# Kernel optimization log

Measured on AMD Instinct MI355X. Metric: run time of the kernel, lower is better.

Reference implementation:

```python
import jax, jax.numpy as jnp
import numpy as np

E = 128          # embed_dim / d_model
DI = 2 * E       # d_inner = expand * d_model = 256
H = 8            # nheads = d_inner / headdim
P = 32           # headdim
N = 64           # d_state
DC = 4           # d_conv
G = 1            # ngroups
XBC = DI + 2 * G * N            # 384
DIN = 2 * DI + 2 * G * N + H    # 648 in_proj width
NL = 4           # number of Mamba2 blocks
PS = 16          # patch size
EPS = 1e-5


def _silu(x):
    return x * jax.nn.sigmoid(x)


def _ln(x, w, b):
    mu = jnp.mean(x, axis=-1, keepdims=True)
    var = jnp.mean(jnp.square(x - mu), axis=-1, keepdims=True)
    return (x - mu) * jax.lax.rsqrt(var + EPS) * w + b


def setup_inputs() -> dict:
    key = jax.random.key(0)
    ks = jax.random.split(key, 20)
    B, IMG = 256, 256
    s = 0.02
    inp = {
        "x": jax.random.normal(ks[0], (B, 3, IMG, IMG), jnp.float32),
        # patch embed conv (E, 3, PS, PS) + bias, then LayerNorm
        "conv_w": jax.random.normal(ks[1], (E, 3, PS, PS), jnp.float32) * s,
        "conv_b": jnp.zeros((E,), jnp.float32),
        "pe_ln_w": jnp.ones((E,), jnp.float32),
        "pe_ln_b": jnp.zeros((E,), jnp.float32),
        # per-block LayerNorms (stacked over NL layers)
        "ln_w": jnp.ones((NL, E), jnp.float32),
        "ln_b": jnp.zeros((NL, E), jnp.float32),
        # Mamba2 params stacked over layers
        "in_w": jax.random.normal(ks[2], (NL, DIN, E), jnp.float32) * s,
        "conv1d_w": jax.random.normal(ks[3], (NL, XBC, DC), jnp.float32) * s,
        "conv1d_b": jnp.zeros((NL, XBC), jnp.float32),
        "dt_bias": jax.random.normal(ks[4], (NL, H), jnp.float32) * 0.5,
        "A_log": jnp.tile(jnp.log(jnp.arange(1, H + 1, dtype=jnp.float32)), (NL, 1)),
        "Dp": jnp.ones((NL, H), jnp.float32),
        "ssm_norm_w": jnp.ones((NL, DI), jnp.float32),
        "out_w": jax.random.normal(ks[5], (NL, E, DI), jnp.float32) * s,
        # final norm + head
        "fn_w": jnp.ones((E,), jnp.float32),
        "fn_b": jnp.zeros((E,), jnp.float32),
        "head_w": jax.random.normal(ks[6], (128, E), jnp.float32) * s,
        "head_b": jnp.zeros((128,), jnp.float32),
    }
    return inp


def _mamba2(x, in_w, cw, cb, dtb, A_log, Dp, nw, ow):
    B, L, _ = x.shape
    zxbcdt = jnp.einsum('ble,de->bld', x, in_w)          # [B,L,648]
    z = zxbcdt[..., :DI]                                  # [B,L,256]
    xbc = zxbcdt[..., DI:DI + XBC]                        # [B,L,384]
    dt = jax.nn.softplus(zxbcdt[..., DI + XBC:] + dtb)    # [B,L,H]
    # causal depthwise conv1d over seq, kernel DC, + silu
    xp = jnp.pad(xbc, ((0, 0), (DC - 1, 0), (0, 0)))
    conv = cb + sum(cw[:, k] * xp[:, k:k + L, :] for k in range(DC))
    xbc = _silu(conv)
    xh = xbc[..., :DI].reshape(B, L, H, P)                # [B,L,H,P]
    Bm = xbc[..., DI:DI + N]                              # [B,L,N] (g=1)
    Cm = xbc[..., DI + N:]                                # [B,L,N]
    A = -jnp.exp(A_log)                                   # [H]
    dA = jnp.exp(dt * A)                                  # [B,L,H]
    # sequential selective scan over L
    def step(h, t):
        dAt, dtt, xt, Bt, Ct = t
        h = dAt[..., None, None] * h + (dtt[..., None] * xt)[..., None] * Bt[:, None, None, :]
        y = jnp.einsum('bhpn,bn->bhp', h, Ct)
        return h, y
    h0 = jnp.zeros((B, H, P, N), x.dtype)
    xs = (jnp.moveaxis(dA, 1, 0), jnp.moveaxis(dt, 1, 0), jnp.moveaxis(xh, 1, 0),
          jnp.moveaxis(Bm, 1, 0), jnp.moveaxis(Cm, 1, 0))
    _, ys = jax.lax.scan(step, h0, xs)                    # [L,B,H,P]
    y = jnp.moveaxis(ys, 0, 1) + Dp[:, None] * xh         # [B,L,H,P]
    y = y.reshape(B, L, DI)
    # gated RMSNorm: rmsnorm(y * silu(z)) * weight
    y = y * _silu(z)
    y = y * jax.lax.rsqrt(jnp.mean(jnp.square(y), axis=-1, keepdims=True) + EPS) * nw
    return jnp.einsum('bld,ed->ble', y, ow)


def reference(x, conv_w, conv_b, pe_ln_w, pe_ln_b, ln_w, ln_b, in_w, conv1d_w,
              conv1d_b, dt_bias, A_log, Dp, ssm_norm_w, out_w, fn_w, fn_b,
              head_w, head_b):
    B = x.shape[0]
    Hh = x.shape[2] // PS
    Ww = x.shape[3] // PS
    # non-overlapping patch conv == blocked einsum
    xp = x.reshape(B, 3, Hh, PS, Ww, PS)
    t = jnp.einsum('bcxpyq,ecpq->bxye', xp, conv_w) + conv_b
    t = t.reshape(B, Hh * Ww, E)                          # [B,L,E]
    t = _ln(t, pe_ln_w, pe_ln_b)
    for i in range(NL):
        t = t + _mamba2(_ln(t, ln_w[i], ln_b[i]), in_w[i], conv1d_w[i],
                        conv1d_b[i], dt_bias[i], A_log[i], Dp[i],
                        ssm_norm_w[i], out_w[i])
    t = _ln(t, fn_w, fn_b)
    t = jnp.mean(t, axis=1)                               # [B,E]
    t = jnp.einsum('be,oe->bo', t, head_w) + head_b       # [B,128]
    nrm = jnp.maximum(jnp.linalg.norm(t, axis=1, keepdims=True), 1e-12)
    return t / nrm
```

## Files before the change

kernel.cpp:

```cpp
#include <hip/hip_runtime.h>
#include <math.h>

#define EE 128
#define DI 256
#define HH 8
#define PP 32
#define NN 64
#define DC 4
#define XBC 384
#define DIN 648
#define NL 4
#define LSEQ 256
#define BB 256
#define TTOK (BB * LSEQ)
#define EPSF 1e-5f

typedef __attribute__((ext_vector_type(8))) short short8;
typedef __attribute__((ext_vector_type(4))) float f32x4;

__device__ inline short f2bf(float f) {
  unsigned u = __builtin_bit_cast(unsigned, f);
  u += 0x7fff + ((u >> 16) & 1);
  return (short)(u >> 16);
}
__device__ inline float bf2f(unsigned short u) {
  unsigned x = ((unsigned)u) << 16;
  return __builtin_bit_cast(float, x);
}
__device__ inline float fast_silu(float a) {
  return a * __builtin_amdgcn_rcpf(1.f + __expf(-a));
}

__global__ __launch_bounds__(256) void cvt_w_kernel(
    const float* __restrict__ in_w, const float* __restrict__ ow,
    unsigned short* __restrict__ in_wb, unsigned short* __restrict__ owb) {
  int i = blockIdx.x * 256 + threadIdx.x;
  in_wb[i] = (unsigned short)f2bf(in_w[i]);
  if (i < NL * EE * DI) owb[i] = (unsigned short)f2bf(ow[i]);
}

__global__ __launch_bounds__(256) void gemm_in_proj(
    const unsigned short* __restrict__ A, const unsigned short* __restrict__ B,
    const unsigned short* __restrict__ Wdt,
    unsigned short* __restrict__ Czx, float* __restrict__ dtraw) {
  __shared__ __align__(16) unsigned short As[128][136];
  __shared__ __align__(16) unsigned short Bs[128][136];
  const int tid = threadIdx.x;
  const int lane = tid & 63, wid = tid >> 6;
  const int wm = wid >> 1, wn = wid & 1;
  const int m0 = blockIdx.y * 128, n0 = blockIdx.x * 128;
  const int r = tid >> 1, hf = tid & 1;
  const int lr = lane & 15, lk = (lane >> 4) * 8;
  {
    const unsigned short* ap = A + (size_t)(m0 + r) * 128 + hf * 64;
#pragma unroll
    for (int v = 0; v < 8; ++v)
      *(short8*)&As[r][hf * 64 + v * 8] = *(const short8*)(ap + v * 8);
    const unsigned short* bp = B + (size_t)(n0 + r) * 128 + hf * 64;
#pragma unroll
    for (int v = 0; v < 8; ++v)
      *(short8*)&Bs[r][hf * 64 + v * 8] = *(const short8*)(bp + v * 8);
  }
  __syncthreads();
  f32x4 acc[4][4] = {};
#pragma unroll
  for (int ks = 0; ks < 4; ++ks) {
    int k0 = ks * 32;
    short8 af[4], bfr[4];
#pragma unroll
    for (int mi = 0; mi < 4; ++mi) af[mi] = *(const short8*)&As[wm * 64 + mi * 16 + lr][k0 + lk];
#pragma unroll
    for (int ni = 0; ni < 4; ++ni) bfr[ni] = *(const short8*)&Bs[wn * 64 + ni * 16 + lr][k0 + lk];
#pragma unroll
    for (int mi = 0; mi < 4; ++mi)
#pragma unroll
      for (int ni = 0; ni < 4; ++ni)
        acc[mi][ni] = __builtin_amdgcn_mfma_f32_16x16x32_bf16(af[mi], bfr[ni], acc[mi][ni], 0, 0, 0);
  }
  if (n0 == 0) {
    f32x4 accd[2] = {};
#pragma unroll
    for (int ks = 0; ks < 4; ++ks) {
      int k0 = ks * 32;
      short8 bw = {};
      if (lr < 8) bw = *(const short8*)(Wdt + (size_t)lr * 128 + k0 + lk);
#pragma unroll
      for (int f = 0; f < 2; ++f) {
        short8 av = *(const short8*)&As[wid * 32 + f * 16 + lr][k0 + lk];
        accd[f] = __builtin_amdgcn_mfma_f32_16x16x32_bf16(av, bw, accd[f], 0, 0, 0);
      }
    }
    if (lr < 8) {
#pragma unroll
      for (int f = 0; f < 2; ++f) {
        int row0 = m0 + wid * 32 + f * 16 + (lane >> 4) * 4;
#pragma unroll
        for (int j = 0; j < 4; ++j)
          dtraw[(size_t)(row0 + j) * 8 + lr] = accd[f][j];
      }
    }
  }
  __syncthreads();
  {
    unsigned short (*Vt)[136] = (unsigned short(*)[136])&As[0][0];
#pragma unroll
    for (int mi = 0; mi < 4; ++mi) {
#pragma unroll
      for (int ni = 0; ni < 4; ++ni) {
        int row0 = wm * 64 + mi * 16 + (lane >> 4) * 4;
        int col = wn * 64 + ni * 16 + lr;
#pragma unroll
        for (int j = 0; j < 4; ++j)
          Vt[row0 + j][col] = (unsigned short)f2bf(acc[mi][ni][j]);
      }
    }
    __syncthreads();
    const int row = tid >> 4, cs = (tid & 15) * 8;
#pragma unroll
    for (int it = 0; it < 8; ++it) {
      int rr2 = it * 16 + row;
      *(uint4*)(Czx + (size_t)(m0 + rr2) * DIN + n0 + cs) = *(const uint4*)&Vt[rr2][cs];
    }
  }
}

__global__ __launch_bounds__(256) void gemm_out_fused_ln(
    const unsigned short* __restrict__ ysc, const unsigned short* __restrict__ zx,
    const float* __restrict__ nw, const unsigned short* __restrict__ B,
    unsigned short* __restrict__ tres, const float* __restrict__ lnw,
    const float* __restrict__ lnb, unsigned* __restrict__ tnb) {
  __shared__ short As[128][40];
  __shared__ short Bs[128][40];
  __shared__ unsigned short Vt[128][136];
  __shared__ float rs_g[128], mu_s[128], rs_s[128];
  const int tid = threadIdx.x;
  const int lane = tid & 63, wid = tid >> 6;
  const int wm = wid >> 1, wn = wid & 1;
  const int m0 = blockIdx.x * 128;
  const int r = tid >> 1, hf = tid & 1;
  const int lr = lane & 15, lk = (lane >> 4) * 8;
  f32x4 acc[4][4] = {};
  float ssg = 0.f;
  for (int k0 = 0; k0 < 256; k0 += 32) {
    {
      int col = k0 + hf * 16;
      const unsigned short* yp = ysc + (size_t)(m0 + r) * DI + col;
      const unsigned short* zp = zx + (size_t)(m0 + r) * DIN + col;
      short8 y0 = *(const short8*)(yp);
      short8 y1 = *(const short8*)(yp + 8);
      short8 z0 = *(const short8*)(zp);
      short8 z1 = *(const short8*)(zp + 8);
      float4 nw0 = *(const float4*)(nw + col);
      float4 nw1 = *(const float4*)(nw + col + 4);
      float4 nw2 = *(const float4*)(nw + col + 8);
      float4 nw3 = *(const float4*)(nw + col + 12);
      float nwv[16] = {nw0.x, nw0.y, nw0.z, nw0.w, nw1.x, nw1.y, nw1.z, nw1.w,
                       nw2.x, nw2.y, nw2.z, nw2.w, nw3.x, nw3.y, nw3.z, nw3.w};
      short8 a0, a1;
#pragma unroll
      for (int j = 0; j < 8; ++j) {
        float y = bf2f((unsigned short)y0[j]);
        float z = bf2f((unsigned short)z0[j]);
        float g = y * fast_silu(z);
        ssg += g * g;
        a0[j] = f2bf(g * nwv[j]);
        float y2 = bf2f((unsigned short)y1[j]);
        float z2 = bf2f((unsigned short)z1[j]);
        float g2 = y2 * fast_silu(z2);
        ssg += g2 * g2;
        a1[j] = f2bf(g2 * nwv[8 + j]);
      }
      *(short8*)&As[r][hf * 16] = a0;
      *(short8*)&As[r][hf * 16 + 8] = a1;
    }
    {
      const unsigned short* bp = B + (size_t)r * 256 + k0 + hf * 16;
      *(short8*)&Bs[r][hf * 16] = *(const short8*)(bp);
      *(short8*)&Bs[r][hf * 16 + 8] = *(const short8*)(bp + 8);
    }
    __syncthreads();
    short8 af[4], bfr[4];
#pragma unroll
    for (int mi = 0; mi < 4; ++mi) af[mi] = *(const short8*)&As[wm * 64 + mi * 16 + lr][lk];
#pragma unroll
    for (int ni = 0; ni < 4; ++ni) bfr[ni] = *(const short8*)&Bs[wn * 64 + ni * 16 + lr][lk];
#pragma unroll
    for (int mi = 0; mi < 4; ++mi)
#pragma unroll
      for (int ni = 0; ni < 4; ++ni)
        acc[mi][ni] = __builtin_amdgcn_mfma_f32_16x16x32_bf16(af[mi], bfr[ni], acc[mi][ni], 0, 0, 0);
    __syncthreads();
  }
  ssg += __shfl_xor(ssg, 1);
  if (hf == 0) rs_g[r] = rsqrtf(ssg * (1.f / 256.f) + EPSF);
  __syncthreads();
#pragma unroll
  for (int mi = 0; mi < 4; ++mi) {
#pragma unroll
    for (int ni = 0; ni < 4; ++ni) {
      int row0 = wm * 64 + mi * 16 + (lane >> 4) * 4;
      int col = wn * 64 + ni * 16 + lr;
#pragma unroll
      for (int j = 0; j < 4; ++j) {
        int row = row0 + j;
        size_t idx = (size_t)(m0 + row) * 128 + col;
        float v = acc[mi][ni][j] * rs_g[row] + bf2f(tres[idx]);
        unsigned short us = (unsigned short)f2bf(v);
        tres[idx] = us;
        Vt[row][col] = us;
      }
    }
  }
  __syncthreads();
  {
    float s = 0.f, ss = 0.f;
#pragma unroll
    for (int kk = 0; kk < 8; ++kk) {
      short8 vv = *(const short8*)&Vt[r][hf * 64 + kk * 8];
#pragma unroll
      for (int j = 0; j < 8; ++j) {
        float f = bf2f((unsigned short)vv[j]);
        s += f; ss += f * f;
      }
    }
    s += __shfl_xor(s, 1);
    ss += __shfl_xor(ss, 1);
    if (hf == 0) {
      float mu = s * (1.f / 128.f);
      mu_s[r] = mu;
      rs_s[r] = rsqrtf(ss * (1.f / 128.f) - mu * mu + EPSF);
    }
  }
  __syncthreads();
  float w0 = lnw[lane * 2], w1 = lnw[lane * 2 + 1];
  float b0 = lnb[lane * 2], b1 = lnb[lane * 2 + 1];
  for (int it = 0; it < 32; ++it) {
    int row = it * 4 + wid;
    float mu = mu_s[row], rr = rs_s[row];
    float v0 = bf2f(Vt[row][lane * 2]);
    float v1 = bf2f(Vt[row][lane * 2 + 1]);
    unsigned lo = (unsigned short)f2bf((v0 - mu) * rr * w0 + b0);
    unsigned hi = (unsigned short)f2bf((v1 - mu) * rr * w1 + b1);
    tnb[(size_t)(m0 + row) * 64 + lane] = lo | (hi << 16);
  }
}

__global__ __launch_bounds__(256) void gemm_bf16_patch(
    const float* __restrict__ X, const float* __restrict__ B,
    const float* __restrict__ bias, unsigned short* __restrict__ C) {
  __shared__ short As[128][40];
  __shared__ short Bs[128][40];
  const int tid = threadIdx.x;
  const int lane = tid & 63, wid = tid >> 6;
  const int wm = wid >> 1, wn = wid & 1;
  const int m0 = blockIdx.x * 128;
  const int r = tid >> 1, hf = tid & 1;
  const int lr = lane & 15, lk = (lane >> 4) * 8;
  const int m = m0 + r;
  const int bb = m >> 8, px = (m >> 4) & 15, py = m & 15;
  f32x4 acc[4][4] = {};
  for (int k0 = 0; k0 < 768; k0 += 32) {
    int k = k0 + hf * 16;
    int c = k >> 8, dx = (k >> 4) & 15;
    {
      const float* ap = X + (((size_t)(bb * 3 + c) * 256 + px * 16 + dx) * 256 + py * 16);
      float4 v0 = *(const float4*)(ap + 0);
      float4 v1 = *(const float4*)(ap + 4);
      float4 v2 = *(const float4*)(ap + 8);
      float4 v3 = *(const float4*)(ap + 12);
      short8 s0, s1;
      s0[0] = f2bf(v0.x); s0[1] = f2bf(v0.y); s0[2] = f2bf(v0.z); s0[3] = f2bf(v0.w);
      s0[4] = f2bf(v1.x); s0[5] = f2bf(v1.y); s0[6] = f2bf(v1.z); s0[7] = f2bf(v1.w);
      s1[0] = f2bf(v2.x); s1[1] = f2bf(v2.y); s1[2] = f2bf(v2.z); s1[3] = f2bf(v2.w);
      s1[4] = f2bf(v3.x); s1[5] = f2bf(v3.y); s1[6] = f2bf(v3.z); s1[7] = f2bf(v3.w);
      *(short8*)&As[r][hf * 16] = s0;
      *(short8*)&As[r][hf * 16 + 8] = s1;
    }
    {
      const float* bp = B + (size_t)r * 768 + k;
      float4 v0 = *(const float4*)(bp + 0);
      float4 v1 = *(const float4*)(bp + 4);
      float4 v2 = *(const float4*)(bp + 8);
      float4 v3 = *(const float4*)(bp + 12);
      short8 s0, s1;
      s0[0] = f2bf(v0.x); s0[1] = f2bf(v0.y); s0[2] = f2bf(v0.z); s0[3] = f2bf(v0.w);
      s0[4] = f2bf(v1.x); s0[5] = f2bf(v1.y); s0[6] = f2bf(v1.z); s0[7] = f2bf(v1.w);
      s1[0] = f2bf(v2.x); s1[1] = f2bf(v2.y); s1[2] = f2bf(v2.z); s1[3] = f2bf(v2.w);
      s1[4] = f2bf(v3.x); s1[5] = f2bf(v3.y); s1[6] = f2bf(v3.z); s1[7] = f2bf(v3.w);
      *(short8*)&Bs[r][hf * 16] = s0;
      *(short8*)&Bs[r][hf * 16 + 8] = s1;
    }
    __syncthreads();
    short8 af[4], bfr[4];
#pragma unroll
    for (int mi = 0; mi < 4; ++mi) af[mi] = *(const short8*)&As[wm * 64 + mi * 16 + lr][lk];
#pragma unroll
    for (int ni = 0; ni < 4; ++ni) bfr[ni] = *(const short8*)&Bs[wn * 64 + ni * 16 + lr][lk];
#pragma unroll
    for (int mi = 0; mi < 4; ++mi)
#pragma unroll
      for (int ni = 0; ni < 4; ++ni)
        acc[mi][ni] = __builtin_amdgcn_mfma_f32_16x16x32_bf16(af[mi], bfr[ni], acc[mi][ni], 0, 0, 0);
    __syncthreads();
  }
#pragma unroll
  for (int mi = 0; mi < 4; ++mi) {
#pragma unroll
    for (int ni = 0; ni < 4; ++ni) {
      int row0 = m0 + wm * 64 + mi * 16 + (lane >> 4) * 4;
      int col = wn * 64 + ni * 16 + (lane & 15);
#pragma unroll
      for (int j = 0; j < 4; ++j)
        C[(size_t)(row0 + j) * 128 + col] = (unsigned short)f2bf(acc[mi][ni][j] + bias[col]);
    }
  }
}

__global__ __launch_bounds__(256) void ln_pe0_kernel(
    unsigned* t, unsigned* out,
    const float* __restrict__ pe_w, const float* __restrict__ pe_b,
    const float* __restrict__ l0w, const float* __restrict__ l0b) {
  int wid = threadIdx.x >> 6, lane = threadIdx.x & 63;
  size_t token = (size_t)blockIdx.x * 4 + wid;
  unsigned* p = t + token * 64;
  unsigned u = p[lane];
  float vx = bf2f((unsigned short)(u & 0xffff));
  float vy = bf2f((unsigned short)(u >> 16));
  float s = vx + vy;
#pragma unroll
  for (int off = 1; off < 64; off <<= 1) s += __shfl_xor(s, off);
  float mu = s * (1.f / 128.f);
  float dx = vx - mu, dy = vy - mu;
  float vs = dx * dx + dy * dy;
#pragma unroll
  for (int off = 1; off < 64; off <<= 1) vs += __shfl_xor(vs, off);
  float r = rsqrtf(vs * (1.f / 128.f) + EPSF);
  float t0 = dx * r * pe_w[lane * 2 + 0] + pe_b[lane * 2 + 0];
  float t1 = dy * r * pe_w[lane * 2 + 1] + pe_b[lane * 2 + 1];
  unsigned short s0 = (unsigned short)f2bf(t0);
  unsigned short s1 = (unsigned short)f2bf(t1);
  p[lane] = (unsigned)s0 | ((unsigned)s1 << 16);
  float r0 = bf2f(s0), r1 = bf2f(s1);
  float s2 = r0 + r1;
#pragma unroll
  for (int off = 1; off < 64; off <<= 1) s2 += __shfl_xor(s2, off);
  float mu2 = s2 * (1.f / 128.f);
  float d0 = r0 - mu2, d1 = r1 - mu2;
  float vs2 = d0 * d0 + d1 * d1;
#pragma unroll
  for (int off = 1; off < 64; off <<= 1) vs2 += __shfl_xor(vs2, off);
  float r2 = rsqrtf(vs2 * (1.f / 128.f) + EPSF);
  unsigned lo = (unsigned short)f2bf(d0 * r2 * l0w[lane * 2 + 0] + l0b[lane * 2 + 0]);
  unsigned hi = (unsigned short)f2bf(d1 * r2 * l0w[lane * 2 + 1] + l0b[lane * 2 + 1]);
  out[token * 64 + lane] = lo | (hi << 16);
}

__global__ __launch_bounds__(256, 2) void scan_chunk_kernel(
    const unsigned short* __restrict__ zx,
    const float* __restrict__ dtraw,
    const float* __restrict__ dtb,
    const float* __restrict__ A_log,
    const float* __restrict__ cw,
    const float* __restrict__ cbv_g,
    const float* __restrict__ Dp,
    unsigned short* __restrict__ ysc) {
  const int b = blockIdx.x & 255, hq = blockIdx.x >> 8;
  const int h0 = hq * 4;
  const int tid = threadIdx.x;
  const int w = tid >> 6, lane = tid & 63;
  const int lr = lane & 15, lj = lane >> 4;
  __shared__ __align__(16) unsigned short Cb[64][72];
  __shared__ __align__(16) unsigned short Bb[64][72];
  __shared__ __align__(16) unsigned short BbT[64][72];
  __shared__ __align__(16) unsigned short Pb[64][72];
  __shared__ __align__(16) unsigned short xT[4][32][72];
  __shared__ __align__(16) unsigned short hbT[4][32][72];
  __shared__ float la[4][64], dtc[4][64], wt[4][64];
  for (int i = tid; i < 4608; i += 256) ((unsigned*)hbT)[i] = 0;
  f32x4 acc_h[8] = {};
  const float dp0 = Dp[h0], dp1 = Dp[h0 + 1], dp2 = Dp[h0 + 2], dp3 = Dp[h0 + 3];
  __syncthreads();

  for (int c = 0; c < 4; ++c) {
    const int tok0 = b * 256 + c * 64;
    {
      int hh = h0 + w;
      float raw = dtraw[(size_t)(tok0 + lane) * 8 + hh] + dtb[hh];
      float dt = raw > 20.f ? raw : log1pf(expf(raw));
      float v = -expf(A_log[hh]) * dt;
#pragma unroll
      for (int off = 1; off < 64; off <<= 1) {
        float u = __shfl_up(v, off);
        if (lane >= off) v += u;
      }
      la[w][lane] = v;
      dtc[w][lane] = dt;
    }
    for (int it = tid; it < 512; it += 256) {
      int t0, ch, kind, sub;
      if (it < 256) {
        int hx = it >> 6, id = it & 63;
        t0 = (id >> 2) * 4; sub = (id & 3) * 8;
        ch = (h0 + hx) * 32 + sub; kind = hx;
      } else if (it < 384) {
        int id = it - 256;
        t0 = (id >> 3) * 4; sub = (id & 7) * 8;
        ch = 256 + sub; kind = 4;
      } else {
        int id = it - 384;
        t0 = (id >> 3) * 4; sub = (id & 7) * 8;
        ch = 320 + sub; kind = 5;
      }
      const unsigned short* zp = zx + (size_t)(tok0 + t0) * DIN + 256 + ch;
      const int t0loc = c * 64 + t0;
      short8 rr[7];
      if (t0loc >= 3) {
#pragma unroll
        for (int d = 0; d < 7; ++d)
          rr[d] = *(const short8*)(zp + (ptrdiff_t)(d - 3) * DIN);
      } else {
#pragma unroll
        for (int d = 0; d < 7; ++d) {
          short8 z8 = {};
          if (t0loc + d - 3 >= 0) z8 = *(const short8*)(zp + (ptrdiff_t)(d - 3) * DIN);
          rr[d] = z8;
        }
      }
      float4 cwv[8];
      float cbl[8];
#pragma unroll
      for (int j = 0; j < 8; ++j) {
        cwv[j] = *(const float4*)(cw + (ch + j) * 4);
        cbl[j] = cbv_g[ch + j];
      }
      short8 o[4];
#pragma unroll
      for (int tt = 0; tt < 4; ++tt) {
#pragma unroll
        for (int j = 0; j < 8; ++j) {
          float a = cbl[j]
                  + cwv[j].x * bf2f((unsigned short)rr[tt + 0][j])
                  + cwv[j].y * bf2f((unsigned short)rr[tt + 1][j])
                  + cwv[j].z * bf2f((unsigned short)rr[tt + 2][j])
                  + cwv[j].w * bf2f((unsigned short)rr[tt + 3][j]);
          o[tt][j] = f2bf(fast_silu(a));
        }
      }
      if (kind < 4) {
#pragma unroll
        for (int j = 0; j < 8; ++j) {
          ushort4 v;
          v.x = (unsigned short)o[0][j]; v.y = (unsigned short)o[1][j];
          v.z = (unsigned short)o[2][j]; v.w = (unsigned short)o[3][j];
          *(ushort4*)&xT[kind][sub + j][t0] = v;
        }
      } else if (kind == 4) {
        *(short8*)&Bb[t0 + 0][sub] = o[0];
        *(short8*)&Bb[t0 + 1][sub] = o[1];
        *(short8*)&Bb[t0 + 2][sub] = o[2];
        *(short8*)&Bb[t0 + 3][sub] = o[3];
#pragma unroll
        for (int j = 0; j < 8; ++j) {
          ushort4 v;
          v.x = (unsigned short)o[0][j]; v.y = (unsigned short)o[1][j];
          v.z = (unsigned short)o[2][j]; v.w = (unsigned short)o[3][j];
          *(ushort4*)&BbT[sub + j][t0] = v;
        }
      } else {
        *(short8*)&Cb[t0 + 0][sub] = o[0];
        *(short8*)&Cb[t0 + 1][sub] = o[1];
        *(short8*)&Cb[t0 + 2][sub] = o[2];
        *(short8*)&Cb[t0 + 3][sub] = o[3];
      }
    }
    __syncthreads();
    wt[w][lane] = __expf(la[w][63] - la[w][lane]) * dtc[w][lane];
    short8 afC0 = *(const short8*)&Cb[w * 16 + lr][lj * 8];
    short8 afC1 = *(const short8*)&Cb[w * 16 + lr][32 + lj * 8];
    f32x4 acc_s[4] = {};
#pragma unroll
    for (int ni = 0; ni < 4; ++ni) {
      short8 bf0 = *(const short8*)&Bb[ni * 16 + lr][lj * 8];
      short8 bf1 = *(const short8*)&Bb[ni * 16 + lr][32 + lj * 8];
      acc_s[ni] = __builtin_amdgcn_mfma_f32_16x16x32_bf16(afC0, bf0, acc_s[ni], 0, 0, 0);
      acc_s[ni] = __builtin_amdgcn_mfma_f32_16x16x32_bf16(afC1, bf1, acc_s[ni], 0, 0, 0);
    }
    f32x4 acc_y[4][2] = {};
#pragma unroll
    for (int hh = 0; hh < 4; ++hh) {
#pragma unroll
      for (int ni = 0; ni < 2; ++ni) {
        short8 hf0 = *(const short8*)&hbT[hh][ni * 16 + lr][lj * 8];
        short8 hf1 = *(const short8*)&hbT[hh][ni * 16 + lr][32 + lj * 8];
        acc_y[hh][ni] = __builtin_amdgcn_mfma_f32_16x16x32_bf16(afC0, hf0, acc_y[hh][ni], 0, 0, 0);
        acc_y[hh][ni] = __builtin_amdgcn_mfma_f32_16x16x32_bf16(afC1, hf1, acc_y[hh][ni], 0, 0, 0);
      }
    }
#pragma unroll
    for (int j = 0; j < 4; ++j) {
      int t = w * 16 + lj * 4 + j;
#pragma unroll
      for (int hh = 0; hh < 4; ++hh) {
        float at = __expf(la[hh][t]);
        acc_y[hh][0][j] *= at;
        acc_y[hh][1][j] *= at;
      }
    }
    {
      float aend = __expf(la[w][63]);
#pragma unroll
      for (int f = 0; f < 8; ++f)
#pragma unroll
        for (int j = 0; j < 4; ++j) acc_h[f][j] *= aend;
#pragma unroll
      for (int kk = 0; kk < 2; ++kk) {
#pragma unroll
        for (int rh = 0; rh < 2; ++rh) {
          short8 xv = *(const short8*)&xT[w][rh * 16 + lr][kk * 32 + lj * 8];
          short8 axf;
#pragma unroll
          for (int j = 0; j < 8; ++j)
            axf[j] = f2bf(bf2f((unsigned short)xv[j]) * wt[w][kk * 32 + lj * 8 + j]);
#pragma unroll
          for (int ni = 0; ni < 4; ++ni) {
            short8 bw = *(const short8*)&BbT[ni * 16 + lr][kk * 32 + lj * 8];
            acc_h[rh * 4 + ni] = __builtin_amdgcn_mfma_f32_16x16x32_bf16(axf, bw, acc_h[rh * 4 + ni], 0, 0, 0);
          }
        }
      }
    }
    __syncthreads();
#pragma unroll
    for (int ni = 0; ni < 4; ++ni) {
      int s = ni * 16 + lr;
      float las0 = la[0][s], dts0 = dtc[0][s];
      float las1 = la[1][s], dts1 = dtc[1][s];
      float las2 = la[2][s], dts2 = dtc[2][s];
      float las3 = la[3][s], dts3 = dtc[3][s];
#pragma unroll
      for (int j = 0; j < 4; ++j) {
        int t = w * 16 + lj * 4 + j;
        float pv0 = 0.f, pv1 = 0.f, pv2 = 0.f, pv3 = 0.f;
        if (s <= t) {
          float sv = acc_s[ni][j];
          pv0 = sv * __expf(la[0][t] - las0) * dts0;
          pv1 = sv * __expf(la[1][t] - las1) * dts1;
          pv2 = sv * __expf(la[2][t] - las2) * dts2;
          pv3 = sv * __expf(la[3][t] - las3) * dts3;
        }
        Cb[t][s]  = (unsigned short)f2bf(pv0);
        Bb[t][s]  = (unsigned short)f2bf(pv1);
        BbT[t][s] = (unsigned short)f2bf(pv2);
        Pb[t][s]  = (unsigned short)f2bf(pv3);
      }
    }
    __syncthreads();
    {
      short8 aP0a = *(const short8*)&Cb[w * 16 + lr][lj * 8];
      short8 aP0b = *(const short8*)&Cb[w * 16 + lr][32 + lj * 8];
      short8 aP1a = *(const short8*)&Bb[w * 16 + lr][lj * 8];
      short8 aP1b = *(const short8*)&Bb[w * 16 + lr][32 + lj * 8];
      short8 aP2a = *(const short8*)&BbT[w * 16 + lr][lj * 8];
      short8 aP2b = *(const short8*)&BbT[w * 16 + lr][32 + lj * 8];
      short8 aP3a = *(const short8*)&Pb[w * 16 + lr][lj * 8];
      short8 aP3b = *(const short8*)&Pb[w * 16 + lr][32 + lj * 8];
#pragma unroll
      for (int ni = 0; ni < 2; ++ni) {
        short8 x0a = *(const short8*)&xT[0][ni * 16 + lr][lj * 8];
        short8 x0b = *(const short8*)&xT[0][ni * 16 + lr][32 + lj * 8];
        acc_y[0][ni] = __builtin_amdgcn_mfma_f32_16x16x32_bf16(aP0a, x0a, acc_y[0][ni], 0, 0, 0);
        acc_y[0][ni] = __builtin_amdgcn_mfma_f32_16x16x32_bf16(aP0b, x0b, acc_y[0][ni], 0, 0, 0);
        short8 x1a = *(const short8*)&xT[1][ni * 16 + lr][lj * 8];
        short8 x1b = *(const short8*)&xT[1][ni * 16 + lr][32 + lj * 8];
        acc_y[1][ni] = __builtin_amdgcn_mfma_f32_16x16x32_bf16(aP1a, x1a, acc_y[1][ni], 0, 0, 0);
        acc_y[1][ni] = __builtin_amdgcn_mfma_f32_16x16x32_bf16(aP1b, x1b, acc_y[1][ni], 0, 0, 0);
        short8 x2a = *(const short8*)&xT[2][ni * 16 + lr][lj * 8];
        short8 x2b = *(const short8*)&xT[2][ni * 16 + lr][32 + lj * 8];
        acc_y[2][ni] = __builtin_amdgcn_mfma_f32_16x16x32_bf16(aP2a, x2a, acc_y[2][ni], 0, 0, 0);
        acc_y[2][ni] = __builtin_amdgcn_mfma_f32_16x16x32_bf16(aP2b, x2b, acc_y[2][ni], 0, 0, 0);
        short8 x3a = *(const short8*)&xT[3][ni * 16 + lr][lj * 8];
        short8 x3b = *(const short8*)&xT[3][ni * 16 + lr][32 + lj * 8];
        acc_y[3][ni] = __builtin_amdgcn_mfma_f32_16x16x32_bf16(aP3a, x3a, acc_y[3][ni], 0, 0, 0);
        acc_y[3][ni] = __builtin_amdgcn_mfma_f32_16x16x32_bf16(aP3b, x3b, acc_y[3][ni], 0, 0, 0);
      }
#pragma unroll
      for (int ni = 0; ni < 2; ++ni) {
#pragma unroll
        for (int j = 0; j < 4; ++j) {
          int t = w * 16 + lj * 4 + j;
          int p = ni * 16 + lr;
          size_t base = (size_t)(tok0 + t) * DI;
          float yv0 = acc_y[0][ni][j] + dp0 * bf2f(xT[0][p][t]);
          ysc[base + (h0 + 0) * 32 + p] = (unsigned short)f2bf(yv0);
          float yv1 = acc_y[1][ni][j] + dp1 * bf2f(xT[1][p][t]);
          ysc[base + (h0 + 1) * 32 + p] = (unsigned short)f2bf(yv1);
          float yv2 = acc_y[2][ni][j] + dp2 * bf2f(xT[2][p][t]);
          ysc[base + (h0 + 2) * 32 + p] = (unsigned short)f2bf(yv2);
          float yv3 = acc_y[3][ni][j] + dp3 * bf2f(xT[3][p][t]);
          ysc[base + (h0 + 3) * 32 + p] = (unsigned short)f2bf(yv3);
        }
      }
    }
#pragma unroll
    for (int rh = 0; rh < 2; ++rh)
#pragma unroll
      for (int ni = 0; ni < 4; ++ni)
#pragma unroll
        for (int j = 0; j < 4; ++j)
          hbT[w][rh * 16 + lj * 4 + j][ni * 16 + lr] = (unsigned short)f2bf(acc_h[rh * 4 + ni][j]);
    __syncthreads();
  }
}

__global__ __launch_bounds__(128) void head_kernel(
    const unsigned short* __restrict__ tn, const float* __restrict__ hw,
    const float* __restrict__ hb, float* __restrict__ out) {
  __shared__ float tm[128];
  __shared__ float red[2];
  int b = blockIdx.x, o = threadIdx.x;
  {
    const unsigned short* p = tn + (size_t)b * 256 * 128 + o;
    float acc = 0.f;
    for (int l = 0; l < 256; ++l) acc += bf2f(p[l * 128]);
    tm[o] = acc * (1.f / 256.f);
  }
  __syncthreads();
  float acc = hb[o];
  for (int e = 0; e < 128; ++e) acc += tm[e] * hw[o * 128 + e];
  float ss = acc * acc;
#pragma unroll
  for (int off = 1; off < 64; off <<= 1) ss += __shfl_xor(ss, off);
  if ((o & 63) == 0) red[o >> 6] = ss;
  __syncthreads();
  float nrm = fmaxf(sqrtf(red[0] + red[1]), 1e-12f);
  out[b * 128 + o] = acc / nrm;
}

extern "C" void kernel_launch(void* const* d_in, const int* in_sizes, int n_in,
                              void* d_out, int out_size, void* d_ws, size_t ws_size,
                              hipStream_t stream) {
  const float* x      = (const float*)d_in[0];
  const float* conv_w = (const float*)d_in[1];
  const float* conv_b = (const float*)d_in[2];
  const float* pe_w   = (const float*)d_in[3];
  const float* pe_b   = (const float*)d_in[4];
  const float* ln_w   = (const float*)d_in[5];
  const float* ln_b   = (const float*)d_in[6];
  const float* in_w   = (const float*)d_in[7];
  const float* c1w    = (const float*)d_in[8];
  const float* c1b    = (const float*)d_in[9];
  const float* dtb    = (const float*)d_in[10];
  const float* A_log  = (const float*)d_in[11];
  const float* Dp     = (const float*)d_in[12];
  const float* nw     = (const float*)d_in[13];
  const float* ow     = (const float*)d_in[14];
  const float* fn_w   = (const float*)d_in[15];
  const float* fn_b   = (const float*)d_in[16];
  const float* hw     = (const float*)d_in[17];
  const float* hb     = (const float*)d_in[18];
  float* out = (float*)d_out;

  const size_t T = TTOK;
  char* w8 = (char*)d_ws;
  unsigned short* t_buf = (unsigned short*)w8;   w8 += T * 128 * 2;
  unsigned*       tnb   = (unsigned*)w8;         w8 += T * 128 * 2;
  unsigned short* zx    = (unsigned short*)w8;   w8 += T * (size_t)DIN * 2;
  float*          dtraw = (float*)w8;            w8 += T * 8 * 4;
  unsigned short* ysc   = (unsigned short*)w8;   w8 += T * (size_t)DI * 2;
  unsigned short* in_wb = (unsigned short*)w8;   w8 += (size_t)NL * DIN * EE * 2;
  unsigned short* owb   = (unsigned short*)w8;   w8 += (size_t)NL * EE * DI * 2;
  if ((size_t)(w8 - (char*)d_ws) > ws_size) return;

  cvt_w_kernel<<<1296, 256, 0, stream>>>(in_w, ow, in_wb, owb);

  gemm_bf16_patch<<<dim3(512, 1), 256, 0, stream>>>(x, conv_w, conv_b, t_buf);
  ln_pe0_kernel<<<16384, 256, 0, stream>>>((unsigned*)t_buf, tnb, pe_w, pe_b, ln_w, ln_b);

  for (int i = 0; i < NL; ++i) {
    gemm_in_proj<<<dim3(5, 512), 256, 0, stream>>>(
        (const unsigned short*)tnb, in_wb + (size_t)i * DIN * EE,
        in_wb + (size_t)i * DIN * EE + 640 * 128, zx, dtraw);
    scan_chunk_kernel<<<512, 256, 0, stream>>>(
        zx, dtraw, dtb + i * HH, A_log + i * HH,
        c1w + (size_t)i * XBC * DC, c1b + (size_t)i * XBC, Dp + i * HH, ysc);
    const float* nlw = (i < NL - 1) ? (ln_w + (i + 1) * 128) : fn_w;
    const float* nlb = (i < NL - 1) ? (ln_b + (i + 1) * 128) : fn_b;
    gemm_out_fused_ln<<<512, 256, 0, stream>>>(
        ysc, zx, nw + i * DI, owb + (size_t)i * EE * DI, t_buf, nlw, nlb, tnb);
  }

  head_kernel<<<256, 128, 0, stream>>>((const unsigned short*)tnb, hw, hb, out);
}
```

Baseline: 546.6 us.

## Double-buffer LDS tiles in out-projection and patch-embed GEMMs

Both the fused out-projection GEMM and the patch-embed GEMM now use two LDS buffers for their A and B tiles. The next K-slice is loaded and converted from global memory into the alternate buffer while MFMAs run on the current one. This hides global-load latency behind compute and drops one barrier per iteration. In exchange the LDS footprint doubles, which may lower occupancy, and the prefetched values add register pressure.

```diff
diff --git a/kernel.cpp b/kernel.cpp
--- a/kernel.cpp
+++ b/kernel.cpp
@@ -129,8 +129,8 @@
     const float* __restrict__ nw, const unsigned short* __restrict__ B,
     unsigned short* __restrict__ tres, const float* __restrict__ lnw,
     const float* __restrict__ lnb, unsigned* __restrict__ tnb) {
-  __shared__ short As[128][40];
-  __shared__ short Bs[128][40];
+  __shared__ short As[2][128][40];
+  __shared__ short Bs[2][128][40];
   __shared__ unsigned short Vt[128][136];
   __shared__ float rs_g[128], mu_s[128], rs_s[128];
   const int tid = threadIdx.x;
@@ -141,49 +141,50 @@
   const int lr = lane & 15, lk = (lane >> 4) * 8;
   f32x4 acc[4][4] = {};
   float ssg = 0.f;
-  for (int k0 = 0; k0 < 256; k0 += 32) {
-    {
-      int col = k0 + hf * 16;
-      const unsigned short* yp = ysc + (size_t)(m0 + r) * DI + col;
-      const unsigned short* zp = zx + (size_t)(m0 + r) * DIN + col;
-      short8 y0 = *(const short8*)(yp);
-      short8 y1 = *(const short8*)(yp + 8);
-      short8 z0 = *(const short8*)(zp);
-      short8 z1 = *(const short8*)(zp + 8);
-      float4 nw0 = *(const float4*)(nw + col);
-      float4 nw1 = *(const float4*)(nw + col + 4);
-      float4 nw2 = *(const float4*)(nw + col + 8);
-      float4 nw3 = *(const float4*)(nw + col + 12);
-      float nwv[16] = {nw0.x, nw0.y, nw0.z, nw0.w, nw1.x, nw1.y, nw1.z, nw1.w,
-                       nw2.x, nw2.y, nw2.z, nw2.w, nw3.x, nw3.y, nw3.z, nw3.w};
-      short8 a0, a1;
-#pragma unroll
-      for (int j = 0; j < 8; ++j) {
-        float y = bf2f((unsigned short)y0[j]);
-        float z = bf2f((unsigned short)z0[j]);
-        float g = y * fast_silu(z);
-        ssg += g * g;
-        a0[j] = f2bf(g * nwv[j]);
-        float y2 = bf2f((unsigned short)y1[j]);
-        float z2 = bf2f((unsigned short)z1[j]);
-        float g2 = y2 * fast_silu(z2);
-        ssg += g2 * g2;
-        a1[j] = f2bf(g2 * nwv[8 + j]);
-      }
-      *(short8*)&As[r][hf * 16] = a0;
-      *(short8*)&As[r][hf * 16 + 8] = a1;
-    }
-    {
-      const unsigned short* bp = B + (size_t)r * 256 + k0 + hf * 16;
-      *(short8*)&Bs[r][hf * 16] = *(const short8*)(bp);
-      *(short8*)&Bs[r][hf * 16 + 8] = *(const short8*)(bp + 8);
-    }
-    __syncthreads();
+  auto stageAB = [&](int ksn, int bufn) {
+    int col = ksn * 32 + hf * 16;
+    const unsigned short* yp = ysc + (size_t)(m0 + r) * DI + col;
+    const unsigned short* zp = zx + (size_t)(m0 + r) * DIN + col;
+    short8 y0 = *(const short8*)(yp);
+    short8 y1 = *(const short8*)(yp + 8);
+    short8 z0 = *(const short8*)(zp);
+    short8 z1 = *(const short8*)(zp + 8);
+    float4 nw0 = *(const float4*)(nw + col);
+    float4 nw1 = *(const float4*)(nw + col + 4);
+    float4 nw2 = *(const float4*)(nw + col + 8);
+    float4 nw3 = *(const float4*)(nw + col + 12);
+    float nwv[16] = {nw0.x, nw0.y, nw0.z, nw0.w, nw1.x, nw1.y, nw1.z, nw1.w,
+                     nw2.x, nw2.y, nw2.z, nw2.w, nw3.x, nw3.y, nw3.z, nw3.w};
+    short8 a0, a1;
+#pragma unroll
+    for (int j = 0; j < 8; ++j) {
+      float y = bf2f((unsigned short)y0[j]);
+      float z = bf2f((unsigned short)z0[j]);
+      float g = y * fast_silu(z);
+      ssg += g * g;
+      a0[j] = f2bf(g * nwv[j]);
+      float y2 = bf2f((unsigned short)y1[j]);
+      float z2 = bf2f((unsigned short)z1[j]);
+      float g2 = y2 * fast_silu(z2);
+      ssg += g2 * g2;
+      a1[j] = f2bf(g2 * nwv[8 + j]);
+    }
+    *(short8*)&As[bufn][r][hf * 16] = a0;
+    *(short8*)&As[bufn][r][hf * 16 + 8] = a1;
+    const unsigned short* bp = B + (size_t)r * 256 + col;
+    *(short8*)&Bs[bufn][r][hf * 16] = *(const short8*)(bp);
+    *(short8*)&Bs[bufn][r][hf * 16 + 8] = *(const short8*)(bp + 8);
+  };
+  stageAB(0, 0);
+  __syncthreads();
+  for (int ks = 0; ks < 8; ++ks) {
+    const int cur = ks & 1;
     short8 af[4], bfr[4];
 #pragma unroll
-    for (int mi = 0; mi < 4; ++mi) af[mi] = *(const short8*)&As[wm * 64 + mi * 16 + lr][lk];
-#pragma unroll
-    for (int ni = 0; ni < 4; ++ni) bfr[ni] = *(const short8*)&Bs[wn * 64 + ni * 16 + lr][lk];
+    for (int mi = 0; mi < 4; ++mi) af[mi] = *(const short8*)&As[cur][wm * 64 + mi * 16 + lr][lk];
+#pragma unroll
+    for (int ni = 0; ni < 4; ++ni) bfr[ni] = *(const short8*)&Bs[cur][wn * 64 + ni * 16 + lr][lk];
+    if (ks < 7) stageAB(ks + 1, cur ^ 1);
 #pragma unroll
     for (int mi = 0; mi < 4; ++mi)
 #pragma unroll
@@ -248,8 +249,8 @@
 __global__ __launch_bounds__(256) void gemm_bf16_patch(
     const float* __restrict__ X, const float* __restrict__ B,
     const float* __restrict__ bias, unsigned short* __restrict__ C) {
-  __shared__ short As[128][40];
-  __shared__ short Bs[128][40];
+  __shared__ short As[2][128][40];
+  __shared__ short Bs[2][128][40];
   const int tid = threadIdx.x;
   const int lane = tid & 63, wid = tid >> 6;
   const int wm = wid >> 1, wn = wid & 1;
@@ -259,8 +260,8 @@
   const int m = m0 + r;
   const int bb = m >> 8, px = (m >> 4) & 15, py = m & 15;
   f32x4 acc[4][4] = {};
-  for (int k0 = 0; k0 < 768; k0 += 32) {
-    int k = k0 + hf * 16;
+  auto stageAB = [&](int ksn, int bufn) {
+    int k = ksn * 32 + hf * 16;
     int c = k >> 8, dx = (k >> 4) & 15;
     {
       const float* ap = X + (((size_t)(bb * 3 + c) * 256 + px * 16 + dx) * 256 + py * 16);
@@ -273,8 +274,8 @@
       s0[4] = f2bf(v1.x); s0[5] = f2bf(v1.y); s0[6] = f2bf(v1.z); s0[7] = f2bf(v1.w);
       s1[0] = f2bf(v2.x); s1[1] = f2bf(v2.y); s1[2] = f2bf(v2.z); s1[3] = f2bf(v2.w);
       s1[4] = f2bf(v3.x); s1[5] = f2bf(v3.y); s1[6] = f2bf(v3.z); s1[7] = f2bf(v3.w);
-      *(short8*)&As[r][hf * 16] = s0;
-      *(short8*)&As[r][hf * 16 + 8] = s1;
+      *(short8*)&As[bufn][r][hf * 16] = s0;
+      *(short8*)&As[bufn][r][hf * 16 + 8] = s1;
     }
     {
       const float* bp = B + (size_t)r * 768 + k;
@@ -287,15 +288,20 @@
       s0[4] = f2bf(v1.x); s0[5] = f2bf(v1.y); s0[6] = f2bf(v1.z); s0[7] = f2bf(v1.w);
       s1[0] = f2bf(v2.x); s1[1] = f2bf(v2.y); s1[2] = f2bf(v2.z); s1[3] = f2bf(v2.w);
       s1[4] = f2bf(v3.x); s1[5] = f2bf(v3.y); s1[6] = f2bf(v3.z); s1[7] = f2bf(v3.w);
-      *(short8*)&Bs[r][hf * 16] = s0;
-      *(short8*)&Bs[r][hf * 16 + 8] = s1;
-    }
-    __syncthreads();
+      *(short8*)&Bs[bufn][r][hf * 16] = s0;
+      *(short8*)&Bs[bufn][r][hf * 16 + 8] = s1;
+    }
+  };
+  stageAB(0, 0);
+  __syncthreads();
+  for (int ks = 0; ks < 24; ++ks) {
+    const int cur = ks & 1;
     short8 af[4], bfr[4];
 #pragma unroll
-    for (int mi = 0; mi < 4; ++mi) af[mi] = *(const short8*)&As[wm * 64 + mi * 16 + lr][lk];
-#pragma unroll
-    for (int ni = 0; ni < 4; ++ni) bfr[ni] = *(const short8*)&Bs[wn * 64 + ni * 16 + lr][lk];
+    for (int mi = 0; mi < 4; ++mi) af[mi] = *(const short8*)&As[cur][wm * 64 + mi * 16 + lr][lk];
+#pragma unroll
+    for (int ni = 0; ni < 4; ++ni) bfr[ni] = *(const short8*)&Bs[cur][wn * 64 + ni * 16 + lr][lk];
+    if (ks < 23) stageAB(ks + 1, cur ^ 1);
 #pragma unroll
     for (int mi = 0; mi < 4; ++mi)
 #pragma unroll
```

After: 558.5 us. +2.2%, slower.
